# Performance work log

Measured on AMD Instinct MI355X. Metric: run time of the kernel, lower is better.

## Reference

```python
import jax, jax.numpy as jnp
import numpy as np

N_WIRES = 4
DIM = 2 ** N_WIRES  # 16-dim statevector


def _zsigns():
    # PauliZ sign per basis state; wire 0 is the most-significant bit
    idx = np.arange(DIM)
    signs = np.stack([1 - 2 * ((idx >> (N_WIRES - 1 - w)) & 1) for w in range(N_WIRES)], 0)
    return jnp.asarray(signs, jnp.float32)  # [4, 16]

ZSIGNS = _zsigns()


def _apply_rx(state, ang, w):
    # state: [B, 16] complex64, ang: [B] rotation angle on wire w
    B = state.shape[0]
    s = state.reshape(B, 2 ** w, 2, 2 ** (N_WIRES - 1 - w))
    c = jnp.cos(ang * 0.5)[:, None, None]
    sn = jnp.sin(ang * 0.5)[:, None, None]
    s0, s1 = s[:, :, 0, :], s[:, :, 1, :]
    o0 = c * s0 - 1j * sn * s1
    o1 = -1j * sn * s0 + c * s1
    return jnp.stack([o0, o1], axis=2).reshape(B, DIM)


def _cnot(state, c, t):
    # flip target bit t where control bit c == 1
    B = state.shape[0]
    s = state.reshape((B,) + (2,) * N_WIRES)
    ca, ta = c + 1, t + 1  # +1 for batch axis
    s0 = jnp.take(s, 0, axis=ca)
    s1 = jnp.take(s, 1, axis=ca)
    t_ax = ta - 1 if ta > ca else ta  # target axis shifts after control axis removed
    s1 = jnp.flip(s1, axis=t_ax)     # size-2 flip == Pauli-X
    return jnp.stack([s0, s1], axis=ca).reshape(B, DIM)


def _qgate(v, theta):
    # v: [B, 4] encoder angles, theta: [4] trainable RX angles (RX angles add)
    B = v.shape[0]
    ang = v + theta[None, :]
    state = jnp.zeros((B, DIM), jnp.complex64).at[:, 0].set(1.0)
    for w in range(N_WIRES):
        state = _apply_rx(state, ang[:, w], w)
    for w in range(N_WIRES):
        state = _cnot(state, w, (w + 1) % N_WIRES)
    probs = jnp.real(state * jnp.conj(state))  # [B, 16]
    return probs @ ZSIGNS.T                    # [B, 4] <Z> per wire


def setup_inputs() -> dict:
    key = jax.random.key(0)
    ks = jax.random.split(key, 16)
    B, S, V, E, H, T = 256, 128, 32000, 256, 4, 32
    d_in = E + H
    sc = 1.0 / np.sqrt(d_in)
    inp = {
        'x': jax.random.randint(ks[0], (B, S), 0, V),
        'embedding': jax.random.normal(ks[1], (V, E), jnp.float32) * 0.02,
        'Wf': jax.random.normal(ks[2], (H, d_in), jnp.float32) * sc,
        'bf': jnp.zeros((H,), jnp.float32),
        'Wi': jax.random.normal(ks[3], (H, d_in), jnp.float32) * sc,
        'bi': jnp.zeros((H,), jnp.float32),
        'Wu': jax.random.normal(ks[4], (H, d_in), jnp.float32) * sc,
        'bu': jnp.zeros((H,), jnp.float32),
        'Wo': jax.random.normal(ks[5], (H, d_in), jnp.float32) * sc,
        'bo': jnp.zeros((H,), jnp.float32),
        'theta_f': jax.random.uniform(ks[6], (H,), jnp.float32, 0.0, 2 * np.pi),
        'theta_i': jax.random.uniform(ks[7], (H,), jnp.float32, 0.0, 2 * np.pi),
        'theta_u': jax.random.uniform(ks[8], (H,), jnp.float32, 0.0, 2 * np.pi),
        'theta_o': jax.random.uniform(ks[9], (H,), jnp.float32, 0.0, 2 * np.pi),
        'Wc': jax.random.normal(ks[10], (T, H), jnp.float32) * 0.5,
        'bc': jnp.zeros((T,), jnp.float32),
    }
    return inp


def reference(x, embedding, Wf, bf, Wi, bi, Wu, bu, Wo, bo,
              theta_f, theta_i, theta_u, theta_o, Wc, bc):
    emb = embedding[x]  # [B, S, E]
    B, S, E = emb.shape
    H = Wf.shape[0]

    def step(carry, xt):
        hx, cx = carry
        comb = jnp.concatenate([xt, hx], axis=1)  # [B, E+H]
        f = jax.nn.sigmoid(_qgate(comb @ Wf.T + bf, theta_f))
        i = jax.nn.sigmoid(_qgate(comb @ Wi.T + bi, theta_i))
        g = jnp.tanh(_qgate(comb @ Wu.T + bu, theta_u))
        o = jax.nn.sigmoid(_qgate(comb @ Wo.T + bo, theta_o))
        cx = f * cx + i * g
        hx = o * jnp.tanh(cx)
        return (hx, cx), hx

    h0 = jnp.zeros((B, H), emb.dtype)
    (_, _), hs = jax.lax.scan(step, (h0, h0), jnp.swapaxes(emb, 0, 1))
    lstm_out = jnp.swapaxes(hs, 0, 1)        # [B, S, H]
    logits = lstm_out @ Wc.T + bc            # [B, S, T]
    return jax.nn.log_softmax(logits, axis=-1)
```

## Files before the change

### kernel.cpp

```cpp
#include <hip/hip_runtime.h>
#include <math.h>

constexpr int NB = 256;
constexpr int NS = 128;
constexpr int NE = 256;
constexpr int DIN = 260;

typedef float f2 __attribute__((ext_vector_type(2)));
#define fma2(A, B, C) __builtin_elementwise_fma((A), (B), (C))

constexpr float INV2PI = 0.15915494309189535f;

__device__ __forceinline__ float rcp_fast(float x) {
#if __has_builtin(__builtin_amdgcn_rcpf)
    return __builtin_amdgcn_rcpf(x);
#else
    return 1.0f / x;
#endif
}

__device__ __forceinline__ float cos_rev(float x) {
    float f, r;
    asm("v_fract_f32 %0, %1" : "=v"(f) : "v"(x));
    asm("v_cos_f32 %0, %1" : "=v"(r) : "v"(f));
    return r;
}

#if __has_builtin(__builtin_amdgcn_mov_dpp)
#define DPP_XOR1(x) __int_as_float(__builtin_amdgcn_mov_dpp(__float_as_int(x), 0xB1, 0xF, 0xF, true))
#define DPP_XOR2(x) __int_as_float(__builtin_amdgcn_mov_dpp(__float_as_int(x), 0x4E, 0xF, 0xF, true))
#define DPP_XOR3(x) __int_as_float(__builtin_amdgcn_mov_dpp(__float_as_int(x), 0x1B, 0xF, 0xF, true))
#else
#define DPP_XOR1(x) __shfl_xor((x), 1, 64)
#define DPP_XOR2(x) __shfl_xor((x), 2, 64)
#define DPP_XOR3(x) __shfl_xor((x), 3, 64)
#endif

__device__ __forceinline__ float tanh_cf(float y) {
    float w = y * y;
    float num = y * fmaf(fmaf(21.0f, w, 1260.0f), w, 10395.0f);
    float den = fmaf(fmaf(w + 210.0f, w, 4725.0f), w, 10395.0f);
    return num * rcp_fast(den);
}

__device__ __forceinline__ float sel4f(float v0, float v1, float v2, float v3,
                                       bool bit0, bool bit1) {
    float lo = bit0 ? v1 : v0;
    float hi = bit0 ? v3 : v2;
    return bit1 ? hi : lo;
}

__device__ __forceinline__ void gload_lds16(const void* gsrc, void* ldst) {
    __builtin_amdgcn_global_load_lds(
        (const __attribute__((address_space(1))) void*)gsrc,
        (__attribute__((address_space(3))) void*)ldst, 16, 0, 0);
}

__global__ __launch_bounds__(256) void k_embed(
    const int* __restrict__ x, const float* __restrict__ emb,
    const float* __restrict__ Wf, const float* __restrict__ bf,
    const float* __restrict__ Wi, const float* __restrict__ bi,
    const float* __restrict__ Wu, const float* __restrict__ bu,
    const float* __restrict__ Wo, const float* __restrict__ bo,
    const float* __restrict__ thf, const float* __restrict__ thi,
    const float* __restrict__ thu, const float* __restrict__ tho,
    float* __restrict__ xpart)
{
    const int lane = threadIdx.x & 63;
    const int wave_id = blockIdx.x * 4 + (threadIdx.x >> 6);

    float4 Wreg[16];
    #pragma unroll
    for (int j = 0; j < 16; ++j) {
        const float* Wgp = (j < 8) ? ((j < 4) ? Wf : Wi) : ((j < 12) ? Wu : Wo);
        float4 w = *(const float4*)(Wgp + (j & 3) * DIN + lane * 4);
        Wreg[j] = make_float4(w.x * INV2PI, w.y * INV2PI, w.z * INV2PI, w.w * INV2PI);
    }
    float biasv;
    {
        int j = lane & 15, jj = j & 3;
        const float* bp = (j < 8) ? ((j < 4) ? bf : bi) : ((j < 12) ? bu : bo);
        const float* tp = (j < 8) ? ((j < 4) ? thf : thi) : ((j < 12) ? thu : tho);
        biasv = (bp[jj] + tp[jj]) * INV2PI;
    }

    const bool p0 = (lane & 1) != 0, p1 = (lane & 2) != 0,
               p2 = (lane & 4) != 0, p3 = (lane & 8) != 0;

    const int row0 = wave_id * 16;

#define LDE(I) (*(const float4*)(emb + \
    (size_t)x[((row0 + (I)) & 255) * NS + ((row0 + (I)) >> 8)] * NE + lane * 4))

#define PROC(I, EV) do {                                                     \
    float acc[16];                                                           \
    _Pragma("unroll")                                                        \
    for (int j = 0; j < 16; ++j) {                                           \
        float4 wv = Wreg[j];                                                 \
        acc[j] = fmaf((EV).x, wv.x, fmaf((EV).y, wv.y,                       \
                  fmaf((EV).z, wv.z, (EV).w * wv.w)));                       \
    }                                                                        \
    float t8[8];                                                             \
    _Pragma("unroll")                                                        \
    for (int i2 = 0; i2 < 8; ++i2) {                                         \
        float keep = p0 ? acc[2 * i2 + 1] : acc[2 * i2];                     \
        float send = p0 ? acc[2 * i2] : acc[2 * i2 + 1];                     \
        t8[i2] = keep + __shfl_xor(send, 1, 64);                             \
    }                                                                        \
    float t4[4];                                                             \
    _Pragma("unroll")                                                        \
    for (int i2 = 0; i2 < 4; ++i2) {                                         \
        float keep = p1 ? t8[2 * i2 + 1] : t8[2 * i2];                       \
        float send = p1 ? t8[2 * i2] : t8[2 * i2 + 1];                       \
        t4[i2] = keep + __shfl_xor(send, 2, 64);                             \
    }                                                                        \
    float t2[2];                                                             \
    _Pragma("unroll")                                                        \
    for (int i2 = 0; i2 < 2; ++i2) {                                         \
        float keep = p2 ? t4[2 * i2 + 1] : t4[2 * i2];                       \
        float send = p2 ? t4[2 * i2] : t4[2 * i2 + 1];                       \
        t2[i2] = keep + __shfl_xor(send, 4, 64);                             \
    }                                                                        \
    float keep = p3 ? t2[1] : t2[0];                                         \
    float send = p3 ? t2[0] : t2[1];                                         \
    float t1 = keep + __shfl_xor(send, 8, 64);                               \
    t1 += __shfl_xor(t1, 16, 64);                                            \
    t1 += __shfl_xor(t1, 32, 64);                                            \
    if (lane < 16)                                                           \
        xpart[(size_t)(row0 + (I)) * 16 + lane] = t1 + biasv;                \
} while (0)

    float4 ev0 = LDE(0), ev1 = LDE(1), ev2 = LDE(2),
           ev3 = LDE(3), ev4 = LDE(4), ev5 = LDE(5);
    PROC(0,  ev0); ev0 = LDE(6);
    PROC(1,  ev1); ev1 = LDE(7);
    PROC(2,  ev2); ev2 = LDE(8);
    PROC(3,  ev3); ev3 = LDE(9);
    PROC(4,  ev4); ev4 = LDE(10);
    PROC(5,  ev5); ev5 = LDE(11);
    PROC(6,  ev0); ev0 = LDE(12);
    PROC(7,  ev1); ev1 = LDE(13);
    PROC(8,  ev2); ev2 = LDE(14);
    PROC(9,  ev3); ev3 = LDE(15);
    PROC(10, ev4);
    PROC(11, ev5);
    PROC(12, ev0);
    PROC(13, ev1);
    PROC(14, ev2);
    PROC(15, ev3);
#undef PROC
#undef LDE
}

__global__ __launch_bounds__(64) void k_recur(
    const float* __restrict__ Wf, const float* __restrict__ Wi,
    const float* __restrict__ Wu, const float* __restrict__ Wo,
    const float* __restrict__ xpart, float* __restrict__ hs)
{
    __shared__ float4 xlds[2][16][64];
    __shared__ float  hlds[128][64];

    const int lane = threadIdx.x;
    const int g = lane & 3;
    const int b0 = blockIdx.x * 16;

    const float* Wg = (g == 0) ? Wf : ((g == 1) ? Wi : ((g == 2) ? Wu : Wo));
    f2 W01[4], W23[4];
    #pragma unroll
    for (int k = 0; k < 4; ++k) {
        W01[k] = f2{Wg[0 * DIN + 256 + (g ^ k)] * INV2PI,
                    Wg[1 * DIN + 256 + (g ^ k)] * INV2PI};
        W23[k] = f2{Wg[2 * DIN + 256 + (g ^ k)] * INV2PI,
                    Wg[3 * DIN + 256 + (g ^ k)] * INV2PI};
    }

    const bool bb0 = (g & 1) != 0, bb1 = (g & 2) != 0;
    const float scl = (g == 2) ? 1.0f : 0.5f;
    const float mlt = (g == 2) ? 1.0f : 0.5f;
    const float bas = (g == 2) ? 0.0f : 0.5f;
    const float s2 = scl * scl;
    const float e0 = mlt * 0.999416f * scl;
    const float e1 = mlt * -0.326958f * scl * s2;
    const float e2 = mlt * 0.111796f * scl * s2 * s2;
    const float e3 = mlt * -0.022660f * scl * s2 * s2 * s2;
    const f2 D0d = {e0, e0}, D1d = {e1, e1}, D2d = {e2, e2}, D3d = {e3, e3};
    const f2 basd = {bas, bas};

    float c = 0.0f;
    float hr0 = 0.f, hr1 = 0.f, hr2 = 0.f, hr3 = 0.f;

    const char* xblk = (const char*)xpart + (size_t)b0 * 64 + (size_t)lane * 16;

    #pragma unroll
    for (int i = 0; i < 16; ++i)
        gload_lds16(xblk + (size_t)i * 16384, &xlds[0][i][0]);
    #pragma unroll
    for (int i = 0; i < 16; ++i)
        gload_lds16(xblk + (size_t)(16 + i) * 16384, &xlds[1][i][0]);
    asm volatile("s_waitcnt vmcnt(16)" ::: "memory");

#define QS(I) do {                                                            \
    float4 xc = xlds[bsel][I][lane];                                          \
    f2 x01 = {xc.x, xc.y}, x23 = {xc.z, xc.w};                                \
    f2 h0d = {hr0, hr0}, h1d = {hr1, hr1}, h2d = {hr2, hr2}, h3d = {hr3, hr3};\
    f2 a01 = fma2(W01[0], h0d, x01);                                          \
    a01 = fma2(W01[1], h1d, a01);                                             \
    a01 = fma2(W01[2], h2d, a01);                                             \
    a01 = fma2(W01[3], h3d, a01);                                             \
    f2 a23 = fma2(W23[0], h0d, x23);                                          \
    a23 = fma2(W23[1], h1d, a23);                                             \
    a23 = fma2(W23[2], h2d, a23);                                             \
    a23 = fma2(W23[3], h3d, a23);                                             \
    float c0_ = cos_rev(a01.x), c1_ = cos_rev(a01.y);                         \
    float c2_ = cos_rev(a23.x), c3_ = cos_rev(a23.y);                         \
    float tt = c2_ * c3_;                                                     \
    float q1 = c0_ * c1_;                                                     \
    f2 q01 = {c1_ * tt, q1};                                                  \
    f2 q23 = {q1 * c2_, q1 * tt};                                             \
    f2 w01 = q01 * q01, w23 = q23 * q23;                                      \
    f2 p01 = fma2(fma2(fma2(D3d, w01, D2d), w01, D1d), w01, D0d);             \
    f2 p23 = fma2(fma2(fma2(D3d, w23, D2d), w23, D1d), w23, D0d);             \
    f2 A01 = fma2(q01, p01, basd);                                            \
    f2 A23 = fma2(q23, p23, basd);                                            \
    float A0 = A01.x, A1 = A01.y, A2 = A23.x, A3 = A23.y;                     \
    float r1 = DPP_XOR1(sel4f(A0, A1, A2, A3, !bb0,  bb1));                   \
    float r2 = DPP_XOR2(sel4f(A0, A1, A2, A3,  bb0, !bb1));                   \
    float r3 = DPP_XOR3(sel4f(A0, A1, A2, A3, !bb0, !bb1));                   \
    float r0 = sel4f(A0, A1, A2, A3, bb0, bb1);                               \
    float fv = sel4f(r0, r1, r2, r3,  bb0,  bb1);                             \
    float iv = sel4f(r0, r1, r2, r3, !bb0,  bb1);                             \
    float uv = sel4f(r0, r1, r2, r3,  bb0, !bb1);                             \
    float ov = sel4f(r0, r1, r2, r3, !bb0, !bb1);                             \
    c = fmaf(fv, c, iv * uv);                                                 \
    float hn = ov * tanh_cf(c);                                               \
    hlds[(cc << 4) + I][lane] = hn;                                           \
    hr0 = hn;                                                                 \
    hr1 = DPP_XOR1(hn);                                                       \
    hr2 = DPP_XOR2(hn);                                                       \
    hr3 = DPP_XOR3(hn);                                                       \
} while (0)

    for (int cc = 0; cc < 8; ++cc) {
        const int bsel = cc & 1;
        QS(0);  QS(1);  QS(2);  QS(3);
        QS(4);  QS(5);  QS(6);  QS(7);
        QS(8);  QS(9);  QS(10); QS(11);
        QS(12); QS(13); QS(14); QS(15);
        if (cc < 6) {
            #pragma unroll
            for (int i = 0; i < 16; ++i)
                gload_lds16(xblk + (size_t)((cc + 2) * 16 + i) * 16384,
                            &xlds[bsel][i][0]);
            asm volatile("s_waitcnt vmcnt(16)" ::: "memory");
        } else if (cc == 6) {
            asm volatile("s_waitcnt vmcnt(0)" ::: "memory");
        }
    }
#undef QS

    #pragma unroll 4
    for (int j = 0; j < 32; ++j) {
        int sp = j * 4 + (lane >> 4);
        float4 v = *(const float4*)&hlds[sp][(lane & 15) * 4];
        *(float4*)(hs + (size_t)sp * 1024 + (size_t)b0 * 4 + (lane & 15) * 4) = v;
    }
}

__global__ __launch_bounds__(256) void k_out(
    const float* __restrict__ hs, const float* __restrict__ Wc,
    const float* __restrict__ bc, float* __restrict__ out)
{
    int gtid = blockIdx.x * 256 + threadIdx.x;
    int r = gtid >> 3;
    int lr = gtid & 7;
    if (r >= NB * NS) return;
    int b = r >> 7, s = r & 127;
    float4 h = *(const float4*)(hs + ((size_t)s * NB + b) * 4);
    float l[4];
    #pragma unroll
    for (int k = 0; k < 4; ++k) {
        int t = lr * 4 + k;
        float4 w = *(const float4*)(Wc + t * 4);
        l[k] = bc[t] + w.x * h.x + w.y * h.y + w.z * h.z + w.w * h.w;
    }
    float m = fmaxf(fmaxf(l[0], l[1]), fmaxf(l[2], l[3]));
    #pragma unroll
    for (int msk = 1; msk < 8; msk <<= 1)
        m = fmaxf(m, __shfl_xor(m, msk, 64));
    float sum = 0.f;
    #pragma unroll
    for (int k = 0; k < 4; ++k)
        sum += __expf(l[k] - m);
    #pragma unroll
    for (int msk = 1; msk < 8; msk <<= 1)
        sum += __shfl_xor(sum, msk, 64);
    float lse = __logf(sum);
    float4 o;
    o.x = l[0] - m - lse;
    o.y = l[1] - m - lse;
    o.z = l[2] - m - lse;
    o.w = l[3] - m - lse;
    *(float4*)(out + (size_t)r * 32 + lr * 4) = o;
}

extern "C" void kernel_launch(void* const* d_in, const int* in_sizes, int n_in,
                              void* d_out, int out_size, void* d_ws, size_t ws_size,
                              hipStream_t stream) {
    const int*   x   = (const int*)d_in[0];
    const float* emb = (const float*)d_in[1];
    const float* Wf  = (const float*)d_in[2];
    const float* bf  = (const float*)d_in[3];
    const float* Wi  = (const float*)d_in[4];
    const float* bi  = (const float*)d_in[5];
    const float* Wu  = (const float*)d_in[6];
    const float* bu  = (const float*)d_in[7];
    const float* Wo  = (const float*)d_in[8];
    const float* bo  = (const float*)d_in[9];
    const float* thf = (const float*)d_in[10];
    const float* thi = (const float*)d_in[11];
    const float* thu = (const float*)d_in[12];
    const float* tho = (const float*)d_in[13];
    const float* Wc  = (const float*)d_in[14];
    const float* bc  = (const float*)d_in[15];
    float* out = (float*)d_out;

    float* xpart = (float*)d_ws;
    float* hs    = xpart + (size_t)NS * NB * 16;

    k_embed<<<512, 256, 0, stream>>>(x, emb, Wf, bf, Wi, bi, Wu, bu, Wo, bo,
                                     thf, thi, thu, tho, xpart);
    k_recur<<<16, 64, 0, stream>>>(Wf, Wi, Wu, Wo, xpart, hs);
    k_out<<<1024, 256, 0, stream>>>(hs, Wc, bc, out);
}
```

Measured before the change: 45.04 us.

## Prefetch recurrence inputs into registers and split gate dot-product dependency chain

Replaces the LDS double-buffered async global-to-LDS prefetch of per-step input projections with a rolling register prefetch of 16 float4 values, loading each slot's next chunk right after it is consumed. This removes LDS reads and the s_waitcnt barriers between chunks from the serial recurrence. The hidden-state FMA chain is also split into two partial sums to shorten the dependent latency on the critical path. It raises VGPR usage and relies on the compiler's waitcnt placement, and the wrapped chunk index makes the last iterations issue redundant loads.

New measurement: 41.39 us (median of 2 runs). -8.1%, faster.

```diff
diff --git a/kernel.cpp b/kernel.cpp
--- a/kernel.cpp
+++ b/kernel.cpp
@@ -48,12 +48,6 @@
     float lo = bit0 ? v1 : v0;
     float hi = bit0 ? v3 : v2;
     return bit1 ? hi : lo;
-}
-
-__device__ __forceinline__ void gload_lds16(const void* gsrc, void* ldst) {
-    __builtin_amdgcn_global_load_lds(
-        (const __attribute__((address_space(1))) void*)gsrc,
-        (__attribute__((address_space(3))) void*)ldst, 16, 0, 0);
 }
 
 __global__ __launch_bounds__(256) void k_embed(
@@ -157,8 +151,7 @@
     const float* __restrict__ Wu, const float* __restrict__ Wo,
     const float* __restrict__ xpart, float* __restrict__ hs)
 {
-    __shared__ float4 xlds[2][16][64];
-    __shared__ float  hlds[128][64];
+    __shared__ float hlds[128][64];
 
     const int lane = threadIdx.x;
     const int g = lane & 3;
@@ -191,26 +184,21 @@
 
     const char* xblk = (const char*)xpart + (size_t)b0 * 64 + (size_t)lane * 16;
 
-    #pragma unroll
-    for (int i = 0; i < 16; ++i)
-        gload_lds16(xblk + (size_t)i * 16384, &xlds[0][i][0]);
-    #pragma unroll
-    for (int i = 0; i < 16; ++i)
-        gload_lds16(xblk + (size_t)(16 + i) * 16384, &xlds[1][i][0]);
-    asm volatile("s_waitcnt vmcnt(16)" ::: "memory");
-
-#define QS(I) do {                                                            \
-    float4 xc = xlds[bsel][I][lane];                                          \
-    f2 x01 = {xc.x, xc.y}, x23 = {xc.z, xc.w};                                \
+#define LDX(CH, K) (*(const float4*)(xblk + (size_t)(((CH) * 8 + (K)) * 16384)))
+
+#define QS(XC, S) do {                                                        \
+    f2 x01 = {(XC).x, (XC).y}, x23 = {(XC).z, (XC).w};                        \
     f2 h0d = {hr0, hr0}, h1d = {hr1, hr1}, h2d = {hr2, hr2}, h3d = {hr3, hr3};\
     f2 a01 = fma2(W01[0], h0d, x01);                                          \
+    f2 n01 = W01[2] * h2d;                                                    \
     a01 = fma2(W01[1], h1d, a01);                                             \
-    a01 = fma2(W01[2], h2d, a01);                                             \
-    a01 = fma2(W01[3], h3d, a01);                                             \
+    n01 = fma2(W01[3], h3d, n01);                                             \
+    a01 = a01 + n01;                                                          \
     f2 a23 = fma2(W23[0], h0d, x23);                                          \
+    f2 n23 = W23[2] * h2d;                                                    \
     a23 = fma2(W23[1], h1d, a23);                                             \
-    a23 = fma2(W23[2], h2d, a23);                                             \
-    a23 = fma2(W23[3], h3d, a23);                                             \
+    n23 = fma2(W23[3], h3d, n23);                                             \
+    a23 = a23 + n23;                                                          \
     float c0_ = cos_rev(a01.x), c1_ = cos_rev(a01.y);                         \
     float c2_ = cos_rev(a23.x), c3_ = cos_rev(a23.y);                         \
     float tt = c2_ * c3_;                                                     \
@@ -233,31 +221,43 @@
     float ov = sel4f(r0, r1, r2, r3, !bb0, !bb1);                             \
     c = fmaf(fv, c, iv * uv);                                                 \
     float hn = ov * tanh_cf(c);                                               \
-    hlds[(cc << 4) + I][lane] = hn;                                           \
+    hlds[S][lane] = hn;                                                       \
     hr0 = hn;                                                                 \
     hr1 = DPP_XOR1(hn);                                                       \
     hr2 = DPP_XOR2(hn);                                                       \
     hr3 = DPP_XOR3(hn);                                                       \
 } while (0)
 
-    for (int cc = 0; cc < 8; ++cc) {
-        const int bsel = cc & 1;
-        QS(0);  QS(1);  QS(2);  QS(3);
-        QS(4);  QS(5);  QS(6);  QS(7);
-        QS(8);  QS(9);  QS(10); QS(11);
-        QS(12); QS(13); QS(14); QS(15);
-        if (cc < 6) {
-            #pragma unroll
-            for (int i = 0; i < 16; ++i)
-                gload_lds16(xblk + (size_t)((cc + 2) * 16 + i) * 16384,
-                            &xlds[bsel][i][0]);
-            asm volatile("s_waitcnt vmcnt(16)" ::: "memory");
-        } else if (cc == 6) {
-            asm volatile("s_waitcnt vmcnt(0)" ::: "memory");
-        }
+    float4 xA0 = LDX(0, 0), xA1 = LDX(0, 1), xA2 = LDX(0, 2), xA3 = LDX(0, 3);
+    float4 xA4 = LDX(0, 4), xA5 = LDX(0, 5), xA6 = LDX(0, 6), xA7 = LDX(0, 7);
+    float4 xB0 = LDX(1, 0), xB1 = LDX(1, 1), xB2 = LDX(1, 2), xB3 = LDX(1, 3);
+    float4 xB4 = LDX(1, 4), xB5 = LDX(1, 5), xB6 = LDX(1, 6), xB7 = LDX(1, 7);
+
+    for (int cp = 0; cp < 8; ++cp) {
+        int s0 = cp * 16;
+        int chA = (cp * 2 + 2) & 15;
+        int chB = (cp * 2 + 3) & 15;
+        QS(xA0, s0 + 0);  xA0 = LDX(chA, 0);
+        QS(xA1, s0 + 1);  xA1 = LDX(chA, 1);
+        QS(xA2, s0 + 2);  xA2 = LDX(chA, 2);
+        QS(xA3, s0 + 3);  xA3 = LDX(chA, 3);
+        QS(xA4, s0 + 4);  xA4 = LDX(chA, 4);
+        QS(xA5, s0 + 5);  xA5 = LDX(chA, 5);
+        QS(xA6, s0 + 6);  xA6 = LDX(chA, 6);
+        QS(xA7, s0 + 7);  xA7 = LDX(chA, 7);
+        QS(xB0, s0 + 8);  xB0 = LDX(chB, 0);
+        QS(xB1, s0 + 9);  xB1 = LDX(chB, 1);
+        QS(xB2, s0 + 10); xB2 = LDX(chB, 2);
+        QS(xB3, s0 + 11); xB3 = LDX(chB, 3);
+        QS(xB4, s0 + 12); xB4 = LDX(chB, 4);
+        QS(xB5, s0 + 13); xB5 = LDX(chB, 5);
+        QS(xB6, s0 + 14); xB6 = LDX(chB, 6);
+        QS(xB7, s0 + 15); xB7 = LDX(chB, 7);
     }
 #undef QS
-
+#undef LDX
+
+    __builtin_amdgcn_s_waitcnt(0);
     #pragma unroll 4
     for (int j = 0; j < 32; ++j) {
         int sp = j * 4 + (lane >> 4);
```
